# Optimization experiments

Measured on AMD Instinct MI355X. Metric: run time of the kernel, lower is better.

## Reference

```python
import jax, jax.numpy as jnp
import numpy as np

MAX_VALUE = 127.0  # 2**(8-1)-1, signed int8 symmetric quantization


def _quantize_int8(t, amax):
    # TensorQuantizer (fake_quant=False): scale = max_value/amax, round, clamp to int8 range.
    s = MAX_VALUE / amax
    return jnp.clip(jnp.round(t * s), -MAX_VALUE, MAX_VALUE)  # integer-valued float32


def setup_inputs() -> dict:
    key = jax.random.key(0)
    kx, kw, kb = jax.random.split(key, 3)
    x = jax.random.normal(kx, (32, 32, 224, 224), dtype=jnp.float32)
    weight = jax.random.normal(kw, (64, 32, 3, 3), dtype=jnp.float32) * 0.06  # kaiming-ish scale
    fan_in = 32 * 3 * 3
    bound = 1.0 / np.sqrt(fan_in)
    bias = jax.random.uniform(kb, (64,), dtype=jnp.float32, minval=-bound, maxval=bound)
    return {"x": x, "weight": weight, "bias": bias}


def reference(x, weight, bias):
    # Calibrated per-tensor amax (histogram calibrator approximated by abs-max)
    amax_x = jax.lax.stop_gradient(jnp.max(jnp.abs(x)))
    amax_w = jax.lax.stop_gradient(jnp.max(jnp.abs(weight)))

    qx = _quantize_int8(x, amax_x)       # int8 values held in fp32
    qw = _quantize_int8(weight, amax_w)

    # Exact int32 systolic conv: accumulation magnitude <= 127*127*288 < 2**24,
    # so fp32 conv reproduces the int32 accumulate bit-exactly.
    out_i32 = jax.lax.conv_general_dilated(
        qx, qw,
        window_strides=(1, 1),
        padding=((1, 1), (1, 1)),
        dimension_numbers=("NCHW", "OIHW", "NCHW"),
        feature_group_count=1,
    )  # [N, Cout, H, W]

    scale = (MAX_VALUE / amax_x) * (MAX_VALUE / amax_w)
    out = out_i32 / scale
    return out + bias[None, :, None, None]
```

## Files before the change

### kernel.cpp

```cpp
#include <hip/hip_runtime.h>
#include <stdint.h>

typedef int v4i __attribute__((ext_vector_type(4)));
typedef float v4f __attribute__((ext_vector_type(4)));

#define BN 32
#define CI 32
#define CO 64
#define HH 224
#define WW 224

#define AMAX_BLOCKS 2048

static const size_t QW_BYTES  = 3 * 64 * 128;
static const size_t AMAX_OFF  = QW_BYTES;

__device__ __forceinline__ int swz(int o) { return o ^ ((o >> 3) & 0x70); }

__global__ __launch_bounds__(256) void k_pre(const float4* __restrict__ x4, long n4,
                                             const float* __restrict__ w,
                                             signed char* __restrict__ qw,
                                             float* __restrict__ amax_pair) {
    int t = threadIdx.x;
    if (blockIdx.x < AMAX_BLOCKS) {
        float m = 0.f;
        long i = (long)blockIdx.x * blockDim.x + t;
        long stride = (long)AMAX_BLOCKS * blockDim.x;
        for (; i < n4; i += stride) {
            float4 v = x4[i];
            m = fmaxf(m, fmaxf(fmaxf(fabsf(v.x), fabsf(v.y)), fmaxf(fabsf(v.z), fabsf(v.w))));
        }
        for (int o = 32; o > 0; o >>= 1) m = fmaxf(m, __shfl_xor(m, o));
        __shared__ float sm[4];
        if ((t & 63) == 0) sm[t >> 6] = m;
        __syncthreads();
        if (t == 0) {
            m = fmaxf(fmaxf(sm[0], sm[1]), fmaxf(sm[2], sm[3]));
            atomicMax((int*)amax_pair, __float_as_int(m));
        }
        return;
    }

    __shared__ __align__(16) signed char qs[24576];
    __shared__ float smw[4];
    __shared__ float s_aw;
    for (int i = t; i < 1536; i += 256) ((v4i*)qs)[i] = (v4i){0, 0, 0, 0};

    float mw = 0.f;
    const float4* w4 = (const float4*)w;
    for (int i = t; i < 4608; i += 256) {
        float4 v = w4[i];
        mw = fmaxf(mw, fmaxf(fmaxf(fabsf(v.x), fabsf(v.y)), fmaxf(fabsf(v.z), fabsf(v.w))));
    }
    for (int o = 32; o > 0; o >>= 1) mw = fmaxf(mw, __shfl_xor(mw, o));
    if ((t & 63) == 0) smw[t >> 6] = mw;
    __syncthreads();
    if (t == 0) {
        s_aw = fmaxf(fmaxf(smw[0], smw[1]), fmaxf(smw[2], smw[3]));
        amax_pair[1] = s_aw;
    }
    __syncthreads();
    float s = 127.0f / s_aw;
    for (int i4 = t; i4 < 4608; i4 += 256) {
        float4 v = w4[i4];
        float e[4] = {v.x, v.y, v.z, v.w};
#pragma unroll
        for (int j = 0; j < 4; j++) {
            int idx = i4 * 4 + j;
            int kw = idx % 3;
            int kh = (idx / 3) % 3;
            int ci = (idx / 9) % 32;
            int o  = idx / 288;
            float q = rintf(e[j] * s);
            q = fminf(127.f, fmaxf(-127.f, q));
            qs[kh * 8192 + o * 128 + kw * 32 + ci] = (signed char)q;
        }
    }
    __syncthreads();
    for (int i = t; i < 1536; i += 256) ((v4i*)qw)[i] = ((const v4i*)qs)[i];
}

__device__ __forceinline__ void qpack_write(const float4 (&v)[4], bool valid, int gh,
                                            int cw, int cbase, float s_x,
                                            signed char* __restrict__ ldsb) {
    int pk[4] = {0, 0, 0, 0};
    if (valid) {
#pragma unroll
        for (int l = 0; l < 4; l++) {
            int q0 = (int)rintf(fminf(127.f, fmaxf(-127.f, v[l].x * s_x)));
            int q1 = (int)rintf(fminf(127.f, fmaxf(-127.f, v[l].y * s_x)));
            int q2 = (int)rintf(fminf(127.f, fmaxf(-127.f, v[l].z * s_x)));
            int q3 = (int)rintf(fminf(127.f, fmaxf(-127.f, v[l].w * s_x)));
            pk[0] |= (q0 & 255) << (8 * l);
            pk[1] |= (q1 & 255) << (8 * l);
            pk[2] |= (q2 & 255) << (8 * l);
            pk[3] |= (q3 & 255) << (8 * l);
        }
    }
#pragma unroll
    for (int j = 0; j < 4; j++)
        *(int*)&ldsb[swz((((gh & 3) * 120) + cw * 4 + j) * 32 + cbase)] = pk[j];
}

__global__ __launch_bounds__(256) void k_conv(const float* __restrict__ x,
                                              const signed char* __restrict__ qw,
                                              const float* __restrict__ bias,
                                              const float* __restrict__ amax_pair,
                                              float* __restrict__ out) {
    __shared__ __align__(16) signed char lds[4 * 120 * 32 + 4 * 16 * 116 * 4];
    float* ep = (float*)(lds + 15360);

    int b = blockIdx.x;
    int wt = b & 1;
    int hs = (b >> 1) & 7;
    int n = b >> 4;
    int w0 = wt * 112;
    int hstart = hs * 28;
    int t = threadIdx.x;
    int lane = t & 63;
    int wv = t >> 6;
    int r = lane & 15;
    int chunk = lane >> 4;
    int cout = wv * 16 + r;

    float ax = __int_as_float(((const int*)amax_pair)[0]);
    float aw = amax_pair[1];
    float s_x = 127.0f / ax;
    float scale = (127.0f / ax) * (127.0f / aw);
    float invs = 1.0f / scale;
    float bv = bias[cout];

    v4i bf[3][2];
#pragma unroll
    for (int dh = 0; dh < 3; dh++)
#pragma unroll
        for (int s = 0; s < 2; s++)
            bf[dh][s] = *(const v4i*)&qw[dh * 8192 + cout * 128 + s * 64 + chunk * 16];

#pragma unroll
    for (int k = 0; k < 4; k++) {
        int task = t + k * 256;
        if (task < 960) {
            int quad = task & 7;
            int rc = task >> 3;
            int cw = rc % 30;
            int row = rc / 30;
            int gh = hstart - 1 + row;
            int gw0 = w0 - 4 + cw * 4;
            int cbase = quad * 4;
            bool valid = ((unsigned)gh < 224u) && ((unsigned)gw0 < 224u);
            float4 v[4];
            if (valid) {
#pragma unroll
                for (int l = 0; l < 4; l++)
                    v[l] = *(const float4*)&x[((size_t)(n * CI + cbase + l) * HH + gh) * WW + gw0];
            }
            qpack_write(v, valid, gh, cw, cbase, s_x, lds);
        }
    }
    __syncthreads();

    float* epw = ep + wv * (16 * 116);

#pragma unroll 1
    for (int i = 0; i < 14; i++) {
        int h0 = hstart + 2 * i;
        bool pf = (i < 13);

        float4 ldA[4], ldB[4];
        int ghA = 0, cwA = 0, cbA = 0, ghB = 0, cwB = 0, cbB = 0;
        bool vA = false, vB = false, hasB = (t < 224);
        if (pf) {
            {
                int task = t;
                int quad = task & 7;
                int rc = task >> 3;
                cwA = rc % 30;
                int row = rc / 30;
                ghA = h0 + 3 + row;
                int gw0 = w0 - 4 + cwA * 4;
                cbA = quad * 4;
                vA = ((unsigned)ghA < 224u) && ((unsigned)gw0 < 224u);
                if (vA) {
#pragma unroll
                    for (int l = 0; l < 4; l++)
                        ldA[l] = *(const float4*)&x[((size_t)(n * CI + cbA + l) * HH + ghA) * WW + gw0];
                }
            }
            if (hasB) {
                int task = t + 256;
                int quad = task & 7;
                int rc = task >> 3;
                cwB = rc % 30;
                int row = rc / 30;
                ghB = h0 + 3 + row;
                int gw0 = w0 - 4 + cwB * 4;
                cbB = quad * 4;
                vB = ((unsigned)ghB < 224u) && ((unsigned)gw0 < 224u);
                if (vB) {
#pragma unroll
                    for (int l = 0; l < 4; l++)
                        ldB[l] = *(const float4*)&x[((size_t)(n * CI + cbB + l) * HH + ghB) * WW + gw0];
                }
            }
        }

        v4i acc[14];
#pragma unroll
        for (int m = 0; m < 14; m++) acc[m] = (v4i){0, 0, 0, 0};
#pragma unroll
        for (int dh = 0; dh < 3; dh++) {
#pragma unroll
            for (int s = 0; s < 2; s++) {
                int k16 = s * 64 + chunk * 16;
                int dw = k16 >> 5;
                if (dw > 2) dw = 2;
                int cih = (k16 >> 4) & 1;
#pragma unroll
                for (int m = 0; m < 14; m++) {
                    int gh = h0 - 1 + (m / 7) + dh;
                    int wl = 3 + (m % 7) * 16 + r + dw;
                    v4i af = *(const v4i*)&lds[swz((((gh & 3) * 120) + wl) * 32 + cih * 16)];
                    acc[m] = __builtin_amdgcn_mfma_i32_16x16x64_i8(af, bf[dh][s], acc[m], 0, 0, 0);
                }
            }
        }

        __syncthreads();

        if (pf) {
            qpack_write(ldA, vA, ghA, cwA, cbA, s_x, lds);
            if (hasB) qpack_write(ldB, vB, ghB, cwB, cbB, s_x, lds);
        }
        __syncthreads();

#pragma unroll
        for (int half = 0; half < 2; half++) {
#pragma unroll
            for (int mm = 0; mm < 7; mm++) {
                int m = half * 7 + mm;
                float4 o;
                o.x = fmaf((float)acc[m][0], invs, bv);
                o.y = fmaf((float)acc[m][1], invs, bv);
                o.z = fmaf((float)acc[m][2], invs, bv);
                o.w = fmaf((float)acc[m][3], invs, bv);
                *(float4*)&epw[r * 116 + mm * 16 + chunk * 4] = o;
            }
            int hh = h0 + half;
#pragma unroll
            for (int it = 0; it < 7; it++) {
                int idx = it * 64 + lane;
                int co = idx / 28;
                int w4i_ = (idx % 28) * 4;
                v4f v = *(const v4f*)&epw[co * 116 + w4i_];
                __builtin_nontemporal_store(v,
                    (v4f*)&out[(((size_t)n * CO + wv * 16 + co) * HH + hh) * WW + w0 + w4i_]);
            }
        }
    }
}

extern "C" void kernel_launch(void* const* d_in, const int* in_sizes, int n_in,
                              void* d_out, int out_size, void* d_ws, size_t ws_size,
                              hipStream_t stream) {
    const float* x = (const float*)d_in[0];
    const float* w = (const float*)d_in[1];
    const float* bias = (const float*)d_in[2];
    float* out = (float*)d_out;

    signed char* qw = (signed char*)d_ws;
    float* amax_pair = (float*)((char*)d_ws + AMAX_OFF);

    long n4 = (long)BN * CI * HH * WW / 4;
    k_pre<<<AMAX_BLOCKS + 1, 256, 0, stream>>>((const float4*)x, n4, w, qw, amax_pair);
    k_conv<<<512, 256, 0, stream>>>(x, qw, bias, amax_pair, out);
}
```

Baseline: 158.8 us.

## Pre-quantize input to NHWC int8 buffer before conv kernel

Adds a separate pass that quantizes x to int8 and writes it channel-last into workspace, after which the conv kernel loads packed int8 rows instead of fp32 NCHW data. This removes the repeated fp32 loads and quantization of halo rows inside the conv loop and cuts its input traffic by about four times. The cost is an extra full read of x plus a write of the int8 copy, and one more launch. The LDS writeback of prefetched rows now runs after the epilogue stores.

```diff
diff --git a/kernel.cpp b/kernel.cpp
--- a/kernel.cpp
+++ b/kernel.cpp
@@ -14,29 +14,67 @@
 
 static const size_t QW_BYTES  = 3 * 64 * 128;
 static const size_t AMAX_OFF  = QW_BYTES;
+static const size_t QX_OFF    = 32768;
 
 __device__ __forceinline__ int swz(int o) { return o ^ ((o >> 3) & 0x70); }
 
-__global__ __launch_bounds__(256) void k_pre(const float4* __restrict__ x4, long n4,
+__global__ __launch_bounds__(256) void k_amax(const float4* __restrict__ x4, long n4,
+                                              float* __restrict__ amax_pair) {
+    int t = threadIdx.x;
+    float m = 0.f;
+    long i = (long)blockIdx.x * blockDim.x + t;
+    long stride = (long)AMAX_BLOCKS * blockDim.x;
+    for (; i < n4; i += stride) {
+        float4 v = x4[i];
+        m = fmaxf(m, fmaxf(fmaxf(fabsf(v.x), fabsf(v.y)), fmaxf(fabsf(v.z), fabsf(v.w))));
+    }
+    for (int o = 32; o > 0; o >>= 1) m = fmaxf(m, __shfl_xor(m, o));
+    __shared__ float sm[4];
+    if ((t & 63) == 0) sm[t >> 6] = m;
+    __syncthreads();
+    if (t == 0) {
+        m = fmaxf(fmaxf(sm[0], sm[1]), fmaxf(sm[2], sm[3]));
+        atomicMax((int*)amax_pair, __float_as_int(m));
+    }
+}
+
+__global__ __launch_bounds__(256) void k_qxw(const float* __restrict__ x,
                                              const float* __restrict__ w,
+                                             signed char* __restrict__ qx,
                                              signed char* __restrict__ qw,
                                              float* __restrict__ amax_pair) {
+    int b = blockIdx.x;
     int t = threadIdx.x;
-    if (blockIdx.x < AMAX_BLOCKS) {
-        float m = 0.f;
-        long i = (long)blockIdx.x * blockDim.x + t;
-        long stride = (long)AMAX_BLOCKS * blockDim.x;
-        for (; i < n4; i += stride) {
-            float4 v = x4[i];
-            m = fmaxf(m, fmaxf(fmaxf(fabsf(v.x), fabsf(v.y)), fmaxf(fabsf(v.z), fabsf(v.w))));
-        }
-        for (int o = 32; o > 0; o >>= 1) m = fmaxf(m, __shfl_xor(m, o));
-        __shared__ float sm[4];
-        if ((t & 63) == 0) sm[t >> 6] = m;
+    if (b < BN * HH) {
+        int h = b % HH;
+        int n = b / HH;
+        float s = 127.0f / __int_as_float(((const int*)amax_pair)[0]);
+        __shared__ signed char ld[CI * 228];
+        const float* xp = x + ((size_t)n * CI * HH + h) * WW;
+        for (int it = 0; it < 7; it++) {
+            int idx = it * 256 + t;
+            int ci = idx / 56;
+            int w0 = (idx % 56) * 4;
+            float4 v = *(const float4*)&xp[(size_t)ci * HH * WW + w0];
+            float q0 = fminf(127.f, fmaxf(-127.f, rintf(v.x * s)));
+            float q1 = fminf(127.f, fmaxf(-127.f, rintf(v.y * s)));
+            float q2 = fminf(127.f, fmaxf(-127.f, rintf(v.z * s)));
+            float q3 = fminf(127.f, fmaxf(-127.f, rintf(v.w * s)));
+            int pk = ((int)q0 & 0xff) | (((int)q1 & 0xff) << 8) |
+                     (((int)q2 & 0xff) << 16) | (((int)q3 & 0xff) << 24);
+            *(int*)&ld[ci * 228 + w0] = pk;
+        }
         __syncthreads();
-        if (t == 0) {
-            m = fmaxf(fmaxf(sm[0], sm[1]), fmaxf(sm[2], sm[3]));
-            atomicMax((int*)amax_pair, __float_as_int(m));
+        int* dst32 = (int*)(qx + ((size_t)n * HH + h) * WW * CI);
+        for (int it = 0; it < 7; it++) {
+            int idx = it * 256 + t;
+            int ww_ = idx >> 3;
+            int cig = idx & 7;
+            int c0 = ld[(cig * 4 + 0) * 228 + ww_] & 0xff;
+            int c1 = ld[(cig * 4 + 1) * 228 + ww_] & 0xff;
+            int c2 = ld[(cig * 4 + 2) * 228 + ww_] & 0xff;
+            int c3 = ld[(cig * 4 + 3) * 228 + ww_] & 0xff;
+            dst32[idx] = c0 | (c1 << 8) | (c2 << 16) | (c3 << 24);
         }
         return;
     }
@@ -80,29 +118,7 @@
     for (int i = t; i < 1536; i += 256) ((v4i*)qw)[i] = ((const v4i*)qs)[i];
 }
 
-__device__ __forceinline__ void qpack_write(const float4 (&v)[4], bool valid, int gh,
-                                            int cw, int cbase, float s_x,
-                                            signed char* __restrict__ ldsb) {
-    int pk[4] = {0, 0, 0, 0};
-    if (valid) {
-#pragma unroll
-        for (int l = 0; l < 4; l++) {
-            int q0 = (int)rintf(fminf(127.f, fmaxf(-127.f, v[l].x * s_x)));
-            int q1 = (int)rintf(fminf(127.f, fmaxf(-127.f, v[l].y * s_x)));
-            int q2 = (int)rintf(fminf(127.f, fmaxf(-127.f, v[l].z * s_x)));
-            int q3 = (int)rintf(fminf(127.f, fmaxf(-127.f, v[l].w * s_x)));
-            pk[0] |= (q0 & 255) << (8 * l);
-            pk[1] |= (q1 & 255) << (8 * l);
-            pk[2] |= (q2 & 255) << (8 * l);
-            pk[3] |= (q3 & 255) << (8 * l);
-        }
-    }
-#pragma unroll
-    for (int j = 0; j < 4; j++)
-        *(int*)&ldsb[swz((((gh & 3) * 120) + cw * 4 + j) * 32 + cbase)] = pk[j];
-}
-
-__global__ __launch_bounds__(256) void k_conv(const float* __restrict__ x,
+__global__ __launch_bounds__(256) void k_conv(const signed char* __restrict__ qx,
                                               const signed char* __restrict__ qw,
                                               const float* __restrict__ bias,
                                               const float* __restrict__ amax_pair,
@@ -125,9 +141,7 @@
 
     float ax = __int_as_float(((const int*)amax_pair)[0]);
     float aw = amax_pair[1];
-    float s_x = 127.0f / ax;
-    float scale = (127.0f / ax) * (127.0f / aw);
-    float invs = 1.0f / scale;
+    float invs = 1.0f / ((127.0f / ax) * (127.0f / aw));
     float bv = bias[cout];
 
     v4i bf[3][2];
@@ -141,21 +155,15 @@
     for (int k = 0; k < 4; k++) {
         int task = t + k * 256;
         if (task < 960) {
-            int quad = task & 7;
-            int rc = task >> 3;
-            int cw = rc % 30;
-            int row = rc / 30;
+            int cih = task & 1;
+            int wl  = (task >> 1) % 120;
+            int row = (task >> 1) / 120;
             int gh = hstart - 1 + row;
-            int gw0 = w0 - 4 + cw * 4;
-            int cbase = quad * 4;
-            bool valid = ((unsigned)gh < 224u) && ((unsigned)gw0 < 224u);
-            float4 v[4];
-            if (valid) {
-#pragma unroll
-                for (int l = 0; l < 4; l++)
-                    v[l] = *(const float4*)&x[((size_t)(n * CI + cbase + l) * HH + gh) * WW + gw0];
-            }
-            qpack_write(v, valid, gh, cw, cbase, s_x, lds);
+            int gw = w0 - 4 + wl;
+            v4i v = (v4i){0, 0, 0, 0};
+            if ((unsigned)gh < 224u && (unsigned)gw < 224u)
+                v = *(const v4i*)&qx[(((size_t)n * HH + gh) * WW + gw) * CI + cih * 16];
+            *(v4i*)&lds[swz((((gh & 3) * 120) + wl) * 32 + cih * 16)] = v;
         }
     }
     __syncthreads();
@@ -167,41 +175,31 @@
         int h0 = hstart + 2 * i;
         bool pf = (i < 13);
 
-        float4 ldA[4], ldB[4];
-        int ghA = 0, cwA = 0, cbA = 0, ghB = 0, cwB = 0, cbB = 0;
-        bool vA = false, vB = false, hasB = (t < 224);
+        v4i ldA = (v4i){0, 0, 0, 0}, ldB = (v4i){0, 0, 0, 0};
+        int shA = 0, shB = 0;
+        bool hasB = (t < 224);
         if (pf) {
             {
                 int task = t;
-                int quad = task & 7;
-                int rc = task >> 3;
-                cwA = rc % 30;
-                int row = rc / 30;
-                ghA = h0 + 3 + row;
-                int gw0 = w0 - 4 + cwA * 4;
-                cbA = quad * 4;
-                vA = ((unsigned)ghA < 224u) && ((unsigned)gw0 < 224u);
-                if (vA) {
-#pragma unroll
-                    for (int l = 0; l < 4; l++)
-                        ldA[l] = *(const float4*)&x[((size_t)(n * CI + cbA + l) * HH + ghA) * WW + gw0];
-                }
+                int cih = task & 1;
+                int wl  = (task >> 1) % 120;
+                int row = (task >> 1) / 120;
+                int gh = h0 + 3 + row;
+                int gw = w0 - 4 + wl;
+                shA = swz((((gh & 3) * 120) + wl) * 32 + cih * 16);
+                if ((unsigned)gh < 224u && (unsigned)gw < 224u)
+                    ldA = *(const v4i*)&qx[(((size_t)n * HH + gh) * WW + gw) * CI + cih * 16];
             }
             if (hasB) {
                 int task = t + 256;
-                int quad = task & 7;
-                int rc = task >> 3;
-                cwB = rc % 30;
-                int row = rc / 30;
-                ghB = h0 + 3 + row;
-                int gw0 = w0 - 4 + cwB * 4;
-                cbB = quad * 4;
-                vB = ((unsigned)ghB < 224u) && ((unsigned)gw0 < 224u);
-                if (vB) {
-#pragma unroll
-                    for (int l = 0; l < 4; l++)
-                        ldB[l] = *(const float4*)&x[((size_t)(n * CI + cbB + l) * HH + ghB) * WW + gw0];
-                }
+                int cih = task & 1;
+                int wl  = (task >> 1) % 120;
+                int row = (task >> 1) / 120;
+                int gh = h0 + 3 + row;
+                int gw = w0 - 4 + wl;
+                shB = swz((((gh & 3) * 120) + wl) * 32 + cih * 16);
+                if ((unsigned)gh < 224u && (unsigned)gw < 224u)
+                    ldB = *(const v4i*)&qx[(((size_t)n * HH + gh) * WW + gw) * CI + cih * 16];
             }
         }
 
@@ -225,14 +223,6 @@
                 }
             }
         }
-
-        __syncthreads();
-
-        if (pf) {
-            qpack_write(ldA, vA, ghA, cwA, cbA, s_x, lds);
-            if (hasB) qpack_write(ldB, vB, ghB, cwB, cbB, s_x, lds);
-        }
-        __syncthreads();
 
 #pragma unroll
         for (int half = 0; half < 2; half++) {
@@ -257,6 +247,14 @@
                     (v4f*)&out[(((size_t)n * CO + wv * 16 + co) * HH + hh) * WW + w0 + w4i_]);
             }
         }
+
+        __syncthreads();
+
+        if (pf) {
+            *(v4i*)&lds[shA] = ldA;
+            if (hasB) *(v4i*)&lds[shB] = ldB;
+        }
+        __syncthreads();
     }
 }
 
@@ -270,8 +268,10 @@
 
     signed char* qw = (signed char*)d_ws;
     float* amax_pair = (float*)((char*)d_ws + AMAX_OFF);
+    signed char* qx = (signed char*)d_ws + QX_OFF;
 
     long n4 = (long)BN * CI * HH * WW / 4;
-    k_pre<<<AMAX_BLOCKS + 1, 256, 0, stream>>>((const float4*)x, n4, w, qw, amax_pair);
-    k_conv<<<512, 256, 0, stream>>>(x, qw, bias, amax_pair, out);
-}
+    k_amax<<<AMAX_BLOCKS, 256, 0, stream>>>((const float4*)x, n4, amax_pair);
+    k_qxw<<<BN * HH + 1, 256, 0, stream>>>(x, w, qx, qw, amax_pair);
+    k_conv<<<512, 256, 0, stream>>>(qx, qw, bias, amax_pair, out);
+}
```

Measured after the change: 189.6 us. 1.19x slower.
